# Optimization experiments

Hardware: AMD Instinct MI355X
Metric: run time of the kernel (lower is better)

Reference implementation:

```python
import jax, jax.numpy as jnp
import numpy as np

GELU = lambda x: jax.nn.gelu(x, approximate=False)  # torch nn.GELU default (erf)
BN_EPS = 1e-5

def _conv(x, w, pad):
    return jax.lax.conv_general_dilated(x, w, (1, 1), pad,
                                        dimension_numbers=('NCHW', 'OIHW', 'NCHW'))

def setup_inputs() -> dict:
    B, D, L = 4096, 768, 3
    IC, R = D // 2, 16  # FDA intermediate channels, reduction ratio
    ks = iter(jax.random.split(jax.random.key(0), 64))
    def nrm(shape, s=0.02):
        return jax.random.normal(next(ks), shape, jnp.float32) * s
    z = lambda *s: jnp.zeros(s, jnp.float32)
    o = lambda *s: jnp.ones(s, jnp.float32)
    inp = {
        'text_feature': jax.random.normal(next(ks), (B, D), jnp.float32),
        'image_feature': jax.random.normal(next(ks), (B, D), jnp.float32),
        'tl_w': nrm((D, D)), 'tl_b': z(D),
        'il_w': nrm((D, D)), 'il_b': z(D),
        'sda_wq': nrm((512, D)), 'sda_bq': z(512),
        'sda_wk': nrm((512, D)), 'sda_bk': z(512),
        'sda_wv': nrm((512, D)), 'sda_bv': z(512),
        'sda_wo': nrm((D, 512)), 'sda_bo': z(D),
        'fda_w1': nrm((IC, D, 3, 3)), 'fda_b1': z(IC),
        'fda_bn1_g': o(IC), 'fda_bn1_b': z(IC),
        'fda_ca_w1': nrm((IC // R, IC, 1, 1)), 'fda_ca_w2': nrm((IC, IC // R, 1, 1)),
        'fda_sa_w': nrm((1, IC, 7, 7)), 'fda_sa_b': z(1),
        'fda_dec_w': nrm((1, IC, 1, 1)), 'fda_dec_b': z(1),
        'fda_sigma': jnp.full((1, IC, 1, 1), 1e-5, jnp.float32),
        'fda_wf': nrm((D, IC, 1, 1)), 'fda_bf': z(D),
        'fda_bn2_g': o(D), 'fda_bn2_b': z(D),
        'dmi_wq': nrm((D, D)), 'dmi_bq': z(D),
        'dmi_wk': nrm((D, D)), 'dmi_bk': z(D),
        'dmi_wv': nrm((D, D)), 'dmi_bv': z(D),
        'tg_w1': nrm((D, D)), 'tg_b1': z(D),
        'tg_w2': nrm((D, D)), 'tg_b2': z(D),
        'ig_w1': nrm((D, D)), 'ig_b1': z(D),
        'ig_w2': nrm((D, D)), 'ig_b2': z(D),
        'text_scale': o(1, D), 'image_scale': o(1, D),
        'cls_w': nrm((L, D)), 'cls_b': z(L),
    }
    return inp

def reference(text_feature, image_feature, tl_w, tl_b, il_w, il_b,
              sda_wq, sda_bq, sda_wk, sda_bk, sda_wv, sda_bv, sda_wo, sda_bo,
              fda_w1, fda_b1, fda_bn1_g, fda_bn1_b, fda_ca_w1, fda_ca_w2,
              fda_sa_w, fda_sa_b, fda_dec_w, fda_dec_b, fda_sigma,
              fda_wf, fda_bf, fda_bn2_g, fda_bn2_b,
              dmi_wq, dmi_bq, dmi_wk, dmi_bk, dmi_wv, dmi_bv,
              tg_w1, tg_b1, tg_w2, tg_b2, ig_w1, ig_b1, ig_w2, ig_b2,
              text_scale, image_scale, cls_w, cls_b):
    B, D = text_feature.shape
    H, DK = 8, 64
    # text/image projections (+GELU; dropout is identity at inference)
    t = GELU(text_feature @ tl_w.T + tl_b)
    im = GELU(image_feature @ il_w.T + il_b)
    # SDA multi-head self-attention on text, seq len 1
    q = (t @ sda_wq.T + sda_bq).reshape(B, 1, H, DK).transpose(0, 2, 1, 3)  # [B,H,1,DK]
    k = (t @ sda_wk.T + sda_bk).reshape(B, 1, H, DK).transpose(0, 2, 1, 3)
    v = (t @ sda_wv.T + sda_bv).reshape(B, 1, H, DK).transpose(0, 2, 1, 3)
    att = jax.nn.softmax(jnp.einsum('bhqd,bhkd->bhqk', q, k) / jnp.sqrt(jnp.float32(DK)), -1)
    t = jnp.einsum('bhqk,bhkd->bhqd', att, v).transpose(0, 2, 1, 3).reshape(B, H * DK) @ sda_wo.T + sda_bo
    # FDA on image feature viewed as [B,C,1,1]
    bnscale = 1.0 / jnp.sqrt(1.0 + BN_EPS)  # BN eval mode, running_mean=0, running_var=1
    x = im[:, :, None, None]
    x = _conv(x, fda_w1, ((1, 1), (1, 1))) + fda_b1[None, :, None, None]
    x = GELU(x * bnscale * fda_bn1_g[None, :, None, None] + fda_bn1_b[None, :, None, None])
    ca = jnp.mean(x, axis=(2, 3), keepdims=True)  # AdaptiveAvgPool2d(1)
    ca = GELU(_conv(ca, fda_ca_w1, ((0, 0), (0, 0))))
    ca = jax.nn.sigmoid(_conv(ca, fda_ca_w2, ((0, 0), (0, 0))))
    x = x * ca
    sa = jax.nn.sigmoid(_conv(x, fda_sa_w, ((3, 3), (3, 3))) + fda_sa_b[None, :, None, None])
    x = x * sa
    xg = GELU(_conv(x, fda_dec_w, ((0, 0), (0, 0))) + fda_dec_b[None, :, None, None])  # [B,1,1,1]
    x = x + fda_sigma * (x - xg)  # feat_decompose residual with learned sigma
    x = _conv(x, fda_wf, ((0, 0), (0, 0))) + fda_bf[None, :, None, None]
    x = GELU(x * bnscale * fda_bn2_g[None, :, None, None] + fda_bn2_b[None, :, None, None])
    im = x[:, :, 0, 0]

    def dmi(q_in, kv_in, gw1, gb1, gw2, gb2, scale):
        qp = q_in @ dmi_wq.T + dmi_bq
        kp = kv_in @ dmi_wk.T + dmi_bk
        vp = kv_in @ dmi_wv.T + dmi_bv
        # cross-batch attention: scores are [B,B]
        a = jax.nn.softmax(qp @ kp.T / jnp.sqrt(jnp.float32(D)), -1) @ vp
        # gate Sequential ends in Sigmoid, then forward applies sigmoid AGAIN (faithful)
        gate = jax.nn.sigmoid(jax.nn.relu(a @ gw1.T + gb1) @ gw2.T + gb2)
        return jax.nn.sigmoid(gate) * a * scale

    ct = dmi(t, im, tg_w1, tg_b1, tg_w2, tg_b2, text_scale)
    ci = dmi(im, t, ig_w1, ig_b1, ig_w2, ig_b2, image_scale)
    logits = (ct + ci) @ cls_w.T + cls_b
    return jax.nn.softmax(logits, -1)
```

## Files before the change

kernel.cpp:

```cpp
#include <hip/hip_runtime.h>
#include <hip/hip_bf16.h>
#include <math.h>

typedef __hip_bfloat16 bf16;
typedef __bf16 bf16x8 __attribute__((ext_vector_type(8)));
typedef float f32x4 __attribute__((ext_vector_type(4)));
typedef unsigned short u16;
typedef u16 u16x8 __attribute__((ext_vector_type(8)));

#define NB 4096
#define DM 768

__device__ __forceinline__ float cvt(float x){ return x; }
__device__ __forceinline__ float cvt(bf16 x){ return __bfloat162float(x); }
__device__ __forceinline__ void stv(float* p, float v){ *p = v; }
__device__ __forceinline__ void stv(bf16* p, float v){ *p = __float2bfloat16(v); }

__device__ __forceinline__ float gelu_f(float x){
    return 0.5f * x * (1.0f + erff(x * 0.70710678118654752440f));
}
__device__ __forceinline__ float sigmoid_f(float x){
    return 1.0f / (1.0f + expf(-x));
}

__device__ __forceinline__ void async_copy16(const void* g, void* l){
    __builtin_amdgcn_global_load_lds((const __attribute__((address_space(1))) void*)g,
                                     (__attribute__((address_space(3))) void*)l, 16, 0, 0);
}

#define MAXJ 8
struct Job {
    const bf16* A; const bf16* B; bf16* C;
    const float* b0; const float* gv; const float* b1;
    int M, N, K, ldA, ldB, act, trans, blk0, nx;
    float alpha;
};
struct Jobs { Job j[MAXJ]; int nj; };

__global__ __launch_bounds__(256) void mgemm_k(Jobs jb)
{
    int z = 0;
    #pragma unroll
    for (int i = 1; i < MAXJ; ++i)
        if (i < jb.nj && (int)blockIdx.x >= jb.j[i].blk0) z = i;
    const Job& J = jb.j[z];
    const bf16* __restrict__ A  = J.A;
    const bf16* __restrict__ Bm = J.B;
    bf16* __restrict__ C        = J.C;
    const int bx = (int)blockIdx.x - J.blk0;
    const int gx = bx % J.nx;
    const int gy = bx / J.nx;
    const int M = J.M, N = J.N, K = J.K, ldA = J.ldA, ldB = J.ldB;

    __shared__ __align__(16) bf16 smem[17408];
    const int tid  = threadIdx.x;
    const int wave = tid >> 6;
    const int lane = tid & 63;
    const int row0 = gy * 128;
    const int col0 = gx * 128;
    const int wrow = (wave & 1) * 64;
    const int wcol = (wave >> 1) * 64;
    const int fl   = lane & 15;
    const int q    = lane >> 4;

    const int sr8 = lane >> 3;
    const int sc8 = (((lane & 7) ^ sr8)) * 8;
    const bf16* pA = A  + (size_t)(row0 + wave * 32 + sr8) * ldA + sc8;
    const bf16* pB = Bm + (size_t)(col0 + wave * 32 + sr8) * ldB + sc8;
    bf16* ldsA = &smem[(wave * 32) * 64];
    bf16* ldsB = &smem[8192 + (wave * 32) * 64];

    f32x4 acc[4][4] = {};
    for (int k0 = 0; k0 < K; k0 += 64){
        #pragma unroll
        for (int i = 0; i < 4; ++i){
            async_copy16(pA + (size_t)(i * 8) * ldA, ldsA + i * 512);
            async_copy16(pB + (size_t)(i * 8) * ldB, ldsB + i * 512);
        }
        pA += 64; pB += 64;
        __syncthreads();
        #pragma unroll
        for (int ks = 0; ks < 2; ++ks){
            bf16x8 af[4], bfv[4];
            #pragma unroll
            for (int i = 0; i < 4; ++i){
                const int ra = wrow + i * 16 + fl;
                const int rb = wcol + i * 16 + fl;
                const int ca = ((ks * 4 + q) ^ (ra & 7)) * 8;
                const int cb = ((ks * 4 + q) ^ (rb & 7)) * 8;
                af[i]  = *(const bf16x8*)&smem[ra * 64 + ca];
                bfv[i] = *(const bf16x8*)&smem[8192 + rb * 64 + cb];
            }
            #pragma unroll
            for (int mi = 0; mi < 4; ++mi)
                #pragma unroll
                for (int ni = 0; ni < 4; ++ni)
                    acc[mi][ni] = __builtin_amdgcn_mfma_f32_16x16x32_bf16(af[mi], bfv[ni], acc[mi][ni], 0, 0, 0);
        }
        __syncthreads();
    }

    constexpr int ELD = 136;
    #pragma unroll
    for (int ni = 0; ni < 4; ++ni){
        const int col = col0 + wcol + ni * 16 + fl;
        const float b0 = J.b0 ? J.b0[col] : 0.f;
        const float gm = (J.gv ? J.gv[col] : 1.f) * J.alpha;
        const float b1 = J.b1 ? J.b1[col] : 0.f;
        const int lcol = wcol + ni * 16 + fl;
        #pragma unroll
        for (int mi = 0; mi < 4; ++mi){
            const int lrow = wrow + mi * 16 + q * 4;
            #pragma unroll
            for (int r = 0; r < 4; ++r){
                float v = (acc[mi][ni][r] + b0) * gm + b1;
                if      (J.act == 1) v = gelu_f(v);
                else if (J.act == 2) v = sigmoid_f(v);
                else if (J.act == 3) v = fmaxf(v, 0.f);
                if (J.trans) smem[(size_t)lcol * ELD + lrow + r] = __float2bfloat16(v);
                else         smem[(size_t)(lrow + r) * ELD + lcol] = __float2bfloat16(v);
            }
        }
    }
    __syncthreads();
    const int erow = tid >> 4;
    const int ecol = (tid & 15) * 8;
    #pragma unroll
    for (int p = 0; p < 8; ++p){
        const int row = p * 16 + erow;
        const bf16x8 val = *(const bf16x8*)&smem[row * ELD + ecol];
        if (J.trans) *(bf16x8*)&C[(size_t)(col0 + row) * M + row0 + ecol] = val;
        else         *(bf16x8*)&C[(size_t)(row0 + row) * N + col0 + ecol] = val;
    }
}

#define NCVT 14
struct CvtDesc { const float* s[NCVT]; bf16* d[NCVT]; int n[NCVT]; };
__global__ __launch_bounds__(256) void cvt_k(CvtDesc cd)
{
    const int e = blockIdx.y;
    const int base = (blockIdx.x * 256 + threadIdx.x) * 4;
    if (base >= cd.n[e]) return;
    const float4 v = *(const float4*)(cd.s[e] + base);
    union { bf16 h[4]; unsigned long long u; } o;
    o.h[0] = __float2bfloat16(v.x);
    o.h[1] = __float2bfloat16(v.y);
    o.h[2] = __float2bfloat16(v.z);
    o.h[3] = __float2bfloat16(v.w);
    *(unsigned long long*)(cd.d[e] + base) = o.u;
}

__global__ __launch_bounds__(256) void extract_k(
    const float* __restrict__ w1, const float* __restrict__ saw,
    bf16* __restrict__ w1c, float* __restrict__ sac)
{
    const int idx = blockIdx.x * 256 + threadIdx.x;
    if (idx < 384 * 768){
        const int oc = idx / 768, ic = idx % 768;
        w1c[idx] = __float2bfloat16(w1[(size_t)oc * 6912 + (size_t)ic * 9 + 4]);
    }
    if (idx < 384) sac[idx] = saw[(size_t)idx * 49 + 24];
}

__global__ __launch_bounds__(128) void fda_fused_k(
    bf16* __restrict__ x, const float* __restrict__ wc1, const float* __restrict__ wc2,
    const float* __restrict__ sac, const float* __restrict__ sab,
    const float* __restrict__ decw, const float* __restrict__ decb,
    const float* __restrict__ sigma)
{
    __shared__ float xs[384];
    __shared__ float ca1s[24];
    __shared__ float red[128];
    const int b = blockIdx.x;
    const int tid = threadIdx.x;
    bf16* xr = x + (size_t)b * 384;
    #pragma unroll
    for (int i = 0; i < 3; ++i) xs[tid + i * 128] = cvt(xr[tid + i * 128]);
    __syncthreads();
    if (tid < 96){
        const int o = tid >> 2, sub = tid & 3;
        const float* w = wc1 + (size_t)o * 384 + sub * 96;
        float p = 0.f;
        #pragma unroll 8
        for (int k = 0; k < 96; ++k) p = fmaf(xs[sub * 96 + k], w[k], p);
        p += __shfl_down(p, 1, 64);
        p += __shfl_down(p, 2, 64);
        if (sub == 0) ca1s[o] = gelu_f(p);
    }
    __syncthreads();
    float x2[3];
    float p = 0.f;
    #pragma unroll
    for (int i = 0; i < 3; ++i){
        const int c = tid + i * 128;
        float s = 0.f;
        const float* w = wc2 + (size_t)c * 24;
        #pragma unroll
        for (int k = 0; k < 24; ++k) s = fmaf(ca1s[k], w[k], s);
        const float v = xs[c] * sigmoid_f(s);
        x2[i] = v;
        p += v * sac[c];
    }
    red[tid] = p; __syncthreads();
    for (int s = 64; s > 0; s >>= 1){ if (tid < s) red[tid] += red[tid + s]; __syncthreads(); }
    const float sa = sigmoid_f(red[0] + sab[0]);
    __syncthreads();
    float qq = 0.f;
    #pragma unroll
    for (int i = 0; i < 3; ++i){
        const int c = tid + i * 128;
        x2[i] *= sa;
        qq += x2[i] * decw[c];
    }
    red[tid] = qq; __syncthreads();
    for (int s = 64; s > 0; s >>= 1){ if (tid < s) red[tid] += red[tid + s]; __syncthreads(); }
    const float xg = gelu_f(red[0] + decb[0]);
    #pragma unroll
    for (int i = 0; i < 3; ++i){
        const int c = tid + i * 128;
        const float sg = sigma[c];
        stv(&xr[c], x2[i] + sg * (x2[i] - xg));
    }
}

__global__ __launch_bounds__(256) void softmax_rows_k(bf16* __restrict__ S)
{
    __shared__ float red[256];
    const int tid = threadIdx.x;
    u16* r = (u16*)(S + (size_t)blockIdx.x * NB) + tid * 16;
    u16x8 h0 = *(const u16x8*)r;
    u16x8 h1 = *(const u16x8*)(r + 8);
    float v[16];
    #pragma unroll
    for (int i = 0; i < 8; ++i){
        v[i]     = __uint_as_float((unsigned)h0[i] << 16);
        v[8 + i] = __uint_as_float((unsigned)h1[i] << 16);
    }
    float m = v[0];
    #pragma unroll
    for (int i = 1; i < 16; ++i) m = fmaxf(m, v[i]);
    red[tid] = m; __syncthreads();
    for (int s = 128; s > 0; s >>= 1){ if (tid < s) red[tid] = fmaxf(red[tid], red[tid + s]); __syncthreads(); }
    m = red[0]; __syncthreads();
    float sum = 0.f;
    #pragma unroll
    for (int i = 0; i < 16; ++i){ v[i] = expf(v[i] - m); sum += v[i]; }
    red[tid] = sum; __syncthreads();
    for (int s = 128; s > 0; s >>= 1){ if (tid < s) red[tid] += red[tid + s]; __syncthreads(); }
    const float inv = 1.0f / red[0];
    u16x8 o0, o1;
    #pragma unroll
    for (int i = 0; i < 8; ++i){
        o0[i] = __bfloat16_as_ushort(__float2bfloat16(v[i] * inv));
        o1[i] = __bfloat16_as_ushort(__float2bfloat16(v[8 + i] * inv));
    }
    *(u16x8*)r = o0;
    *(u16x8*)(r + 8) = o1;
}

__global__ __launch_bounds__(256) void reduce2_k(
    const bf16* __restrict__ a, const bf16* __restrict__ b, bf16* __restrict__ o1,
    const bf16* __restrict__ c, const bf16* __restrict__ d, bf16* __restrict__ o2)
{
    const size_t i = ((size_t)blockIdx.x * 256 + threadIdx.x) * 8;
    if (i >= (size_t)NB * DM) return;
    u16x8 ua = *(const u16x8*)((const u16*)a + i);
    u16x8 ub = *(const u16x8*)((const u16*)b + i);
    u16x8 uc = *(const u16x8*)((const u16*)c + i);
    u16x8 ud = *(const u16x8*)((const u16*)d + i);
    u16x8 r1, r2;
    #pragma unroll
    for (int j = 0; j < 8; ++j){
        const float s1 = __uint_as_float((unsigned)ua[j] << 16) + __uint_as_float((unsigned)ub[j] << 16);
        const float s2 = __uint_as_float((unsigned)uc[j] << 16) + __uint_as_float((unsigned)ud[j] << 16);
        r1[j] = __bfloat16_as_ushort(__float2bfloat16(s1));
        r2[j] = __bfloat16_as_ushort(__float2bfloat16(s2));
    }
    *(u16x8*)((u16*)o1 + i) = r1;
    *(u16x8*)((u16*)o2 + i) = r2;
}

__global__ __launch_bounds__(256) void combine2_k(
    bf16* __restrict__ acc,
    const bf16* __restrict__ g1, const bf16* __restrict__ a1, const float* __restrict__ s1,
    const bf16* __restrict__ g2, const bf16* __restrict__ a2, const float* __restrict__ s2)
{
    const size_t idx = (size_t)blockIdx.x * 256 + threadIdx.x;
    if (idx >= (size_t)NB * DM) return;
    const int col = (int)(idx % DM);
    const float v = sigmoid_f(cvt(g1[idx])) * cvt(a1[idx]) * s1[col]
                  + sigmoid_f(cvt(g2[idx])) * cvt(a2[idx]) * s2[col];
    stv(&acc[idx], v);
}

__global__ __launch_bounds__(64) void cls_softmax_k(
    const bf16* __restrict__ acc, const float* __restrict__ w,
    const float* __restrict__ bias, float* __restrict__ out)
{
    const int b = blockIdx.x;
    const bf16* r = acc + (size_t)b * DM;
    float p0 = 0.f, p1 = 0.f, p2 = 0.f;
    for (int k = threadIdx.x; k < DM; k += 64){
        const float v = cvt(r[k]);
        p0 = fmaf(v, w[k],        p0);
        p1 = fmaf(v, w[DM + k],   p1);
        p2 = fmaf(v, w[2*DM + k], p2);
    }
    #pragma unroll
    for (int off = 32; off > 0; off >>= 1){
        p0 += __shfl_down(p0, off, 64);
        p1 += __shfl_down(p1, off, 64);
        p2 += __shfl_down(p2, off, 64);
    }
    if (threadIdx.x == 0){
        const float l0 = p0 + bias[0];
        const float l1 = p1 + bias[1];
        const float l2 = p2 + bias[2];
        const float mx = fmaxf(l0, fmaxf(l1, l2));
        const float e0 = expf(l0 - mx), e1 = expf(l1 - mx), e2 = expf(l2 - mx);
        const float inv = 1.f / (e0 + e1 + e2);
        out[(size_t)b * 3 + 0] = e0 * inv;
        out[(size_t)b * 3 + 1] = e1 * inv;
        out[(size_t)b * 3 + 2] = e2 * inv;
    }
}

extern "C" void kernel_launch(void* const* d_in, const int* in_sizes, int n_in,
                              void* d_out, int out_size, void* d_ws, size_t ws_size,
                              hipStream_t stream)
{
    const float* text   = (const float*)d_in[0];
    const float* image  = (const float*)d_in[1];
    const float* tl_w   = (const float*)d_in[2];
    const float* tl_b   = (const float*)d_in[3];
    const float* il_w   = (const float*)d_in[4];
    const float* il_b   = (const float*)d_in[5];
    const float* sda_wv = (const float*)d_in[10];
    const float* sda_bv = (const float*)d_in[11];
    const float* sda_wo = (const float*)d_in[12];
    const float* sda_bo = (const float*)d_in[13];
    const float* fda_w1 = (const float*)d_in[14];
    const float* fda_b1 = (const float*)d_in[15];
    const float* bn1_g  = (const float*)d_in[16];
    const float* bn1_b  = (const float*)d_in[17];
    const float* ca_w1  = (const float*)d_in[18];
    const float* ca_w2  = (const float*)d_in[19];
    const float* sa_w   = (const float*)d_in[20];
    const float* sa_b   = (const float*)d_in[21];
    const float* dec_w  = (const float*)d_in[22];
    const float* dec_b  = (const float*)d_in[23];
    const float* sigma  = (const float*)d_in[24];
    const float* fda_wf = (const float*)d_in[25];
    const float* fda_bf = (const float*)d_in[26];
    const float* bn2_g  = (const float*)d_in[27];
    const float* bn2_b  = (const float*)d_in[28];
    const float* dmi_wq = (const float*)d_in[29];
    const float* dmi_bq = (const float*)d_in[30];
    const float* dmi_wk = (const float*)d_in[31];
    const float* dmi_bk = (const float*)d_in[32];
    const float* dmi_wv = (const float*)d_in[33];
    const float* dmi_bv = (const float*)d_in[34];
    const float* tg_w1  = (const float*)d_in[35];
    const float* tg_b1  = (const float*)d_in[36];
    const float* tg_w2  = (const float*)d_in[37];
    const float* tg_b2  = (const float*)d_in[38];
    const float* ig_w1  = (const float*)d_in[39];
    const float* ig_b1  = (const float*)d_in[40];
    const float* ig_w2  = (const float*)d_in[41];
    const float* ig_b2  = (const float*)d_in[42];
    const float* t_scale= (const float*)d_in[43];
    const float* i_scale= (const float*)d_in[44];
    const float* cls_w  = (const float*)d_in[45];
    const float* cls_b  = (const float*)d_in[46];
    float* out = (float*)d_out;

    char* base = (char*)d_ws;
    auto alloc = [&](size_t bytes){ void* p = (void*)base; base += (bytes + 255) & ~(size_t)255; return p; };
    const size_t SLOT = (size_t)NB * DM;
    const size_t W768 = (size_t)768 * 768;
    bf16* tl_wb   = (bf16*)alloc(W768 * 2);
    bf16* il_wb   = (bf16*)alloc(W768 * 2);
    bf16* sda_wvb = (bf16*)alloc((size_t)512 * 768 * 2);
    bf16* sda_wob = (bf16*)alloc((size_t)768 * 512 * 2);
    bf16* fda_wfb = (bf16*)alloc((size_t)768 * 384 * 2);
    bf16* dmi_wqb = (bf16*)alloc(W768 * 2);
    bf16* dmi_wkb = (bf16*)alloc(W768 * 2);
    bf16* dmi_wvb = (bf16*)alloc(W768 * 2);
    bf16* tg_w1b  = (bf16*)alloc(W768 * 2);
    bf16* tg_w2b  = (bf16*)alloc(W768 * 2);
    bf16* ig_w1b  = (bf16*)alloc(W768 * 2);
    bf16* ig_w2b  = (bf16*)alloc(W768 * 2);
    bf16* w1c     = (bf16*)alloc((size_t)384 * 768 * 2);
    float* sac    = (float*)alloc(1536 * 4);
    bf16* SL[8];
    for (int i = 0; i < 8; ++i) SL[i] = (bf16*)alloc(SLOT * 2);
    bf16* SC1 = (bf16*)alloc((size_t)NB * NB * 2);
    bf16* SC2 = (bf16*)alloc((size_t)NB * NB * 2);

    const float bnscale = 1.0f / sqrtf(1.0f + 1e-5f);
    const float iscale  = 1.0f / sqrtf(768.0f);
    const dim3 blk(256);

    struct JB {
        Jobs jb; int blocks;
        void add(const bf16* A, const bf16* B, bf16* C, int M, int N, int K, int ldA, int ldB,
                 const float* b0, float al, const float* gv, const float* b1, int act, int trans){
            Job& j = jb.j[jb.nj++];
            j.A=A; j.B=B; j.C=C; j.b0=b0; j.gv=gv; j.b1=b1;
            j.M=M; j.N=N; j.K=K; j.ldA=ldA; j.ldB=ldB; j.act=act; j.trans=trans;
            j.alpha=al; j.blk0=blocks; j.nx=N/128;
            blocks += (N/128)*(M/128);
        }
    };
    auto launch = [&](JB& b){ mgemm_k<<<dim3(b.blocks), blk, 0, stream>>>(b.jb); };

    CvtDesc cd;
    const float* srcs[NCVT] = {text, image, tl_w, il_w, sda_wv, sda_wo, fda_wf,
                               dmi_wq, dmi_wk, dmi_wv, tg_w1, tg_w2, ig_w1, ig_w2};
    bf16* dsts[NCVT] = {SL[0], SL[1], tl_wb, il_wb, sda_wvb, sda_wob, fda_wfb,
                        dmi_wqb, dmi_wkb, dmi_wvb, tg_w1b, tg_w2b, ig_w1b, ig_w2b};
    int   lens[NCVT] = {(int)SLOT, (int)SLOT, (int)W768, (int)W768, 512*768, 768*512, 768*384,
                        (int)W768, (int)W768, (int)W768, (int)W768, (int)W768, (int)W768, (int)W768};
    for (int i = 0; i < NCVT; ++i){ cd.s[i] = srcs[i]; cd.d[i] = dsts[i]; cd.n[i] = lens[i]; }
    cvt_k<<<dim3((int)(SLOT / 1024), NCVT), blk, 0, stream>>>(cd);
    extract_k<<<dim3((384 * 768 + 255) / 256), blk, 0, stream>>>(fda_w1, sa_w, w1c, sac);

    { JB b{}; b.add(SL[0], tl_wb, SL[2], NB, DM, DM, DM, DM, tl_b, 1.f, nullptr, nullptr, 1, 0);
              b.add(SL[1], il_wb, SL[3], NB, DM, DM, DM, DM, il_b, 1.f, nullptr, nullptr, 1, 0); launch(b); }
    { JB b{}; b.add(SL[2], sda_wvb, SL[0], NB, 512, DM, DM, DM, sda_bv, 1.f, nullptr, nullptr, 0, 0);
              b.add(SL[3], w1c,     SL[1], NB, 384, DM, DM, DM, fda_b1, bnscale, bn1_g, bn1_b, 1, 0); launch(b); }
    { JB b{}; b.add(SL[0], sda_wob, SL[4], NB, DM, 512, 512, 512, sda_bo, 1.f, nullptr, nullptr, 0, 0); launch(b); }
    fda_fused_k<<<dim3(NB), dim3(128), 0, stream>>>(SL[1], ca_w1, ca_w2, sac, sa_b, dec_w, dec_b, sigma);
    { JB b{}; b.add(SL[1], fda_wfb, SL[5], NB, DM, 384, 384, 384, fda_bf, bnscale, bn2_g, bn2_b, 1, 0); launch(b); }

    { JB b{};
      b.add(SL[4], dmi_wqb, SL[0], NB, DM, DM, DM, DM, dmi_bq, 1.f, nullptr, nullptr, 0, 0);
      b.add(SL[5], dmi_wkb, SL[1], NB, DM, DM, DM, DM, dmi_bk, 1.f, nullptr, nullptr, 0, 0);
      b.add(SL[5], dmi_wvb, SL[2], NB, DM, DM, DM, DM, dmi_bv, 1.f, nullptr, nullptr, 0, 1);
      b.add(SL[5], dmi_wqb, SL[3], NB, DM, DM, DM, DM, dmi_bq, 1.f, nullptr, nullptr, 0, 0);
      b.add(SL[4], dmi_wkb, SL[6], NB, DM, DM, DM, DM, dmi_bk, 1.f, nullptr, nullptr, 0, 0);
      b.add(SL[4], dmi_wvb, SL[7], NB, DM, DM, DM, DM, dmi_bv, 1.f, nullptr, nullptr, 0, 1);
      launch(b); }
    { JB b{}; b.add(SL[0], SL[1], SC1, NB, NB, DM, DM, DM, nullptr, iscale, nullptr, nullptr, 0, 0);
              b.add(SL[3], SL[6], SC2, NB, NB, DM, DM, DM, nullptr, iscale, nullptr, nullptr, 0, 0); launch(b); }
    softmax_rows_k<<<dim3(2 * NB), blk, 0, stream>>>(SC1);
    { JB b{};
      b.add(SC1,        SL[2],        SL[0], NB, DM, 2048, NB, NB, nullptr, 1.f, nullptr, nullptr, 0, 0);
      b.add(SC1 + 2048, SL[2] + 2048, SL[1], NB, DM, 2048, NB, NB, nullptr, 1.f, nullptr, nullptr, 0, 0);
      b.add(SC2,        SL[7],        SL[3], NB, DM, 2048, NB, NB, nullptr, 1.f, nullptr, nullptr, 0, 0);
      b.add(SC2 + 2048, SL[7] + 2048, SL[6], NB, DM, 2048, NB, NB, nullptr, 1.f, nullptr, nullptr, 0, 0);
      launch(b); }
    reduce2_k<<<dim3((int)(SLOT / 2048)), blk, 0, stream>>>(SL[0], SL[1], SL[4], SL[3], SL[6], SL[5]);
    { JB b{}; b.add(SL[4], tg_w1b, SL[0], NB, DM, DM, DM, DM, tg_b1, 1.f, nullptr, nullptr, 3, 0);
              b.add(SL[5], ig_w1b, SL[1], NB, DM, DM, DM, DM, ig_b1, 1.f, nullptr, nullptr, 3, 0); launch(b); }
    { JB b{}; b.add(SL[0], tg_w2b, SL[3], NB, DM, DM, DM, DM, tg_b2, 1.f, nullptr, nullptr, 2, 0);
              b.add(SL[1], ig_w2b, SL[6], NB, DM, DM, DM, DM, ig_b2, 1.f, nullptr, nullptr, 2, 0); launch(b); }
    combine2_k<<<dim3((NB * DM + 255) / 256), blk, 0, stream>>>(SL[2], SL[3], SL[4], t_scale, SL[6], SL[5], i_scale);
    cls_softmax_k<<<dim3(NB), dim3(64), 0, stream>>>(SL[2], cls_w, cls_b, out);
}
```

Measured before the change: 600.4 us.

## Fuse exp into score GEMM epilogue and defer softmax normalization

The score GEMM epilogue now applies exp directly, with no row-max subtraction. A small kernel then computes per-row sums of the exponentiated scores, and the division by the row sum moves into the reduce kernel that runs after the attention-value GEMM. This removes the separate softmax pass that read and rewrote both 4096x4096 score matrices, leaving only a read pass for the sums. The sda_wo and fda_wf GEMMs are also batched into one launch after fda_fused_k to improve GPU fill. Skipping max subtraction risks overflow or precision loss if the scores grow large.

```diff
diff --git a/kernel.cpp b/kernel.cpp
--- a/kernel.cpp
+++ b/kernel.cpp
@@ -117,6 +117,7 @@
                 if      (J.act == 1) v = gelu_f(v);
                 else if (J.act == 2) v = sigmoid_f(v);
                 else if (J.act == 3) v = fmaxf(v, 0.f);
+                else if (J.act == 4) v = expf(v);
                 if (J.trans) smem[(size_t)lcol * ELD + lrow + r] = __float2bfloat16(v);
                 else         smem[(size_t)(lrow + r) * ELD + lcol] = __float2bfloat16(v);
             }
@@ -223,47 +224,35 @@
     }
 }
 
-__global__ __launch_bounds__(256) void softmax_rows_k(bf16* __restrict__ S)
+__global__ __launch_bounds__(256) void rowsum_k(const bf16* __restrict__ S, float* __restrict__ l)
 {
     __shared__ float red[256];
     const int tid = threadIdx.x;
-    u16* r = (u16*)(S + (size_t)blockIdx.x * NB) + tid * 16;
+    const u16* r = (const u16*)(S + (size_t)blockIdx.x * NB) + tid * 16;
     u16x8 h0 = *(const u16x8*)r;
     u16x8 h1 = *(const u16x8*)(r + 8);
-    float v[16];
+    float sum = 0.f;
     #pragma unroll
     for (int i = 0; i < 8; ++i){
-        v[i]     = __uint_as_float((unsigned)h0[i] << 16);
-        v[8 + i] = __uint_as_float((unsigned)h1[i] << 16);
-    }
-    float m = v[0];
-    #pragma unroll
-    for (int i = 1; i < 16; ++i) m = fmaxf(m, v[i]);
-    red[tid] = m; __syncthreads();
-    for (int s = 128; s > 0; s >>= 1){ if (tid < s) red[tid] = fmaxf(red[tid], red[tid + s]); __syncthreads(); }
-    m = red[0]; __syncthreads();
-    float sum = 0.f;
-    #pragma unroll
-    for (int i = 0; i < 16; ++i){ v[i] = expf(v[i] - m); sum += v[i]; }
+        sum += __uint_as_float((unsigned)h0[i] << 16);
+        sum += __uint_as_float((unsigned)h1[i] << 16);
+    }
     red[tid] = sum; __syncthreads();
     for (int s = 128; s > 0; s >>= 1){ if (tid < s) red[tid] += red[tid + s]; __syncthreads(); }
-    const float inv = 1.0f / red[0];
-    u16x8 o0, o1;
-    #pragma unroll
-    for (int i = 0; i < 8; ++i){
-        o0[i] = __bfloat16_as_ushort(__float2bfloat16(v[i] * inv));
-        o1[i] = __bfloat16_as_ushort(__float2bfloat16(v[8 + i] * inv));
-    }
-    *(u16x8*)r = o0;
-    *(u16x8*)(r + 8) = o1;
+    if (tid == 0) l[blockIdx.x] = red[0];
 }
 
 __global__ __launch_bounds__(256) void reduce2_k(
     const bf16* __restrict__ a, const bf16* __restrict__ b, bf16* __restrict__ o1,
-    const bf16* __restrict__ c, const bf16* __restrict__ d, bf16* __restrict__ o2)
+    const float* __restrict__ l1,
+    const bf16* __restrict__ c, const bf16* __restrict__ d, bf16* __restrict__ o2,
+    const float* __restrict__ l2)
 {
     const size_t i = ((size_t)blockIdx.x * 256 + threadIdx.x) * 8;
     if (i >= (size_t)NB * DM) return;
+    const int row = (int)(i / DM);
+    const float inv1 = 1.0f / l1[row];
+    const float inv2 = 1.0f / l2[row];
     u16x8 ua = *(const u16x8*)((const u16*)a + i);
     u16x8 ub = *(const u16x8*)((const u16*)b + i);
     u16x8 uc = *(const u16x8*)((const u16*)c + i);
@@ -271,8 +260,8 @@
     u16x8 r1, r2;
     #pragma unroll
     for (int j = 0; j < 8; ++j){
-        const float s1 = __uint_as_float((unsigned)ua[j] << 16) + __uint_as_float((unsigned)ub[j] << 16);
-        const float s2 = __uint_as_float((unsigned)uc[j] << 16) + __uint_as_float((unsigned)ud[j] << 16);
+        const float s1 = (__uint_as_float((unsigned)ua[j] << 16) + __uint_as_float((unsigned)ub[j] << 16)) * inv1;
+        const float s2 = (__uint_as_float((unsigned)uc[j] << 16) + __uint_as_float((unsigned)ud[j] << 16)) * inv2;
         r1[j] = __bfloat16_as_ushort(__float2bfloat16(s1));
         r2[j] = __bfloat16_as_ushort(__float2bfloat16(s2));
     }
@@ -392,6 +381,7 @@
     bf16* ig_w2b  = (bf16*)alloc(W768 * 2);
     bf16* w1c     = (bf16*)alloc((size_t)384 * 768 * 2);
     float* sac    = (float*)alloc(1536 * 4);
+    float* lbuf   = (float*)alloc(2 * NB * 4);
     bf16* SL[8];
     for (int i = 0; i < 8; ++i) SL[i] = (bf16*)alloc(SLOT * 2);
     bf16* SC1 = (bf16*)alloc((size_t)NB * NB * 2);
@@ -429,9 +419,9 @@
               b.add(SL[1], il_wb, SL[3], NB, DM, DM, DM, DM, il_b, 1.f, nullptr, nullptr, 1, 0); launch(b); }
     { JB b{}; b.add(SL[2], sda_wvb, SL[0], NB, 512, DM, DM, DM, sda_bv, 1.f, nullptr, nullptr, 0, 0);
               b.add(SL[3], w1c,     SL[1], NB, 384, DM, DM, DM, fda_b1, bnscale, bn1_g, bn1_b, 1, 0); launch(b); }
-    { JB b{}; b.add(SL[0], sda_wob, SL[4], NB, DM, 512, 512, 512, sda_bo, 1.f, nullptr, nullptr, 0, 0); launch(b); }
     fda_fused_k<<<dim3(NB), dim3(128), 0, stream>>>(SL[1], ca_w1, ca_w2, sac, sa_b, dec_w, dec_b, sigma);
-    { JB b{}; b.add(SL[1], fda_wfb, SL[5], NB, DM, 384, 384, 384, fda_bf, bnscale, bn2_g, bn2_b, 1, 0); launch(b); }
+    { JB b{}; b.add(SL[0], sda_wob, SL[4], NB, DM, 512, 512, 512, sda_bo, 1.f, nullptr, nullptr, 0, 0);
+              b.add(SL[1], fda_wfb, SL[5], NB, DM, 384, 384, 384, fda_bf, bnscale, bn2_g, bn2_b, 1, 0); launch(b); }
 
     { JB b{};
       b.add(SL[4], dmi_wqb, SL[0], NB, DM, DM, DM, DM, dmi_bq, 1.f, nullptr, nullptr, 0, 0);
@@ -441,16 +431,17 @@
       b.add(SL[4], dmi_wkb, SL[6], NB, DM, DM, DM, DM, dmi_bk, 1.f, nullptr, nullptr, 0, 0);
       b.add(SL[4], dmi_wvb, SL[7], NB, DM, DM, DM, DM, dmi_bv, 1.f, nullptr, nullptr, 0, 1);
       launch(b); }
-    { JB b{}; b.add(SL[0], SL[1], SC1, NB, NB, DM, DM, DM, nullptr, iscale, nullptr, nullptr, 0, 0);
-              b.add(SL[3], SL[6], SC2, NB, NB, DM, DM, DM, nullptr, iscale, nullptr, nullptr, 0, 0); launch(b); }
-    softmax_rows_k<<<dim3(2 * NB), blk, 0, stream>>>(SC1);
+    { JB b{}; b.add(SL[0], SL[1], SC1, NB, NB, DM, DM, DM, nullptr, iscale, nullptr, nullptr, 4, 0);
+              b.add(SL[3], SL[6], SC2, NB, NB, DM, DM, DM, nullptr, iscale, nullptr, nullptr, 4, 0); launch(b); }
+    rowsum_k<<<dim3(2 * NB), blk, 0, stream>>>(SC1, lbuf);
     { JB b{};
       b.add(SC1,        SL[2],        SL[0], NB, DM, 2048, NB, NB, nullptr, 1.f, nullptr, nullptr, 0, 0);
       b.add(SC1 + 2048, SL[2] + 2048, SL[1], NB, DM, 2048, NB, NB, nullptr, 1.f, nullptr, nullptr, 0, 0);
       b.add(SC2,        SL[7],        SL[3], NB, DM, 2048, NB, NB, nullptr, 1.f, nullptr, nullptr, 0, 0);
       b.add(SC2 + 2048, SL[7] + 2048, SL[6], NB, DM, 2048, NB, NB, nullptr, 1.f, nullptr, nullptr, 0, 0);
       launch(b); }
-    reduce2_k<<<dim3((int)(SLOT / 2048)), blk, 0, stream>>>(SL[0], SL[1], SL[4], SL[3], SL[6], SL[5]);
+    reduce2_k<<<dim3((int)(SLOT / 2048)), blk, 0, stream>>>(SL[0], SL[1], SL[4], lbuf,
+                                                           SL[3], SL[6], SL[5], lbuf + NB);
     { JB b{}; b.add(SL[4], tg_w1b, SL[0], NB, DM, DM, DM, DM, tg_b1, 1.f, nullptr, nullptr, 3, 0);
               b.add(SL[5], ig_w1b, SL[1], NB, DM, DM, DM, DM, ig_b1, 1.f, nullptr, nullptr, 3, 0); launch(b); }
     { JB b{}; b.add(SL[0], tg_w2b, SL[3], NB, DM, DM, DM, DM, tg_b2, 1.f, nullptr, nullptr, 2, 0);
```

After: 600.1 us. About the same (-0.0%).
